# Optimization experiments

Measured on AMD Instinct MI355X. Metric: run time of the kernel, lower is better.

## Reference

```python
import jax, jax.numpy as jnp
import numpy as np

TEMPERATURE = 0.7
TOP_K = 50
TOP_P = 0.9
B, S, H, V = 2, 1024, 512, 50257


def setup_inputs() -> dict:
    key = jax.random.key(0)
    k1, k2 = jax.random.split(key)
    x = jax.random.normal(k1, (B, S, H), dtype=jnp.float32)
    # small init scale keeps logits in a realistic range so nucleus mass is spread
    W = jax.random.normal(k2, (V, H), dtype=jnp.float32) * 0.02
    b = jnp.zeros((V,), dtype=jnp.float32)
    return {"x": x, "W": W, "b": b}


def _top_k_top_p_filtering(logits):
    # --- top-k: mask everything below the k-th largest value ---
    top_k_vals = jax.lax.top_k(logits, TOP_K)[0]          # [B,S,K]
    min_top_k = top_k_vals[..., -1:]                       # [B,S,1]
    logits = jnp.where(logits < min_top_k, -jnp.inf, logits)
    # --- top-p (nucleus): sort descending, cumsum of probs, drop tail ---
    sorted_idx = jnp.argsort(-logits, axis=-1)             # descending order
    sorted_logits = jnp.take_along_axis(logits, sorted_idx, axis=-1)
    cum_probs = jnp.cumsum(jax.nn.softmax(sorted_logits, axis=-1), axis=-1)
    sorted_logits = jnp.where(cum_probs > TOP_P, -jnp.inf, sorted_logits)
    # NOTE: the original torch code does gather(sorted_logits, index=sorted_indices)
    # (forward-gather, not inverse scatter). We replicate that exact math.
    logits = jnp.take_along_axis(sorted_logits, sorted_idx, axis=-1)
    return logits


def reference(x, W, b):
    # ExampleModel: single linear projection to vocab logits [B,S,V]
    logits = jnp.einsum('bsh,vh->bsv', x, W) + b
    logits = logits / TEMPERATURE
    filtered = _top_k_top_p_filtering(logits)
    return jax.nn.softmax(filtered, axis=-1)
```

## Files before the change

### kernel.cpp

```cpp
#include <hip/hip_runtime.h>
#include <math.h>

#define TEMP 0.7f
#define TOPK 50
#define TOPP 0.9f
#define M_TOT 2048
#define K_DIM 512
#define V_DIM 50257
#define NPAD 50304
#define KP 1536
#define BM 256
#define BN 128
#define BKE 64
#define NSTEP (KP / BKE)
#define NBN (NPAD / BN)
#define NBM (M_TOT / BM)

typedef short s16x8 __attribute__((ext_vector_type(8)));
typedef float f32x4 __attribute__((ext_vector_type(4)));

#define MFMA_16x16x32_BF16(acc, va, vb) \
  asm("v_mfma_f32_16x16x32_bf16 %0, %1, %2, %0" : "+v"(acc) : "v"(va), "v"(vb))

__device__ __forceinline__ unsigned short bf16_rn(float x) {
  unsigned u = __float_as_uint(x);
  unsigned r = u + 0x7FFFu + ((u >> 16) & 1u);
  return (unsigned short)(r >> 16);
}
__device__ __forceinline__ float bf16_to_f(unsigned short h) {
  return __uint_as_float(((unsigned)h) << 16);
}
__device__ __forceinline__ unsigned f2key(float f) {
  unsigned u = __float_as_uint(f);
  return (u & 0x80000000u) ? ~u : (u | 0x80000000u);
}

#define NQX (M_TOT * (K_DIM / 4))
#define NQW (NPAD * (K_DIM / 4))
#define NZQ ((M_TOT * V_DIM) / 4)

__global__ __launch_bounds__(256) void conv_kernel(const float* __restrict__ X,
                                                   const float* __restrict__ W,
                                                   unsigned short* __restrict__ Xp,
                                                   unsigned short* __restrict__ Wp,
                                                   float* __restrict__ Z, int nzq) {
  int idx = blockIdx.x * 256 + threadIdx.x;
  if (idx >= NQX + NQW) {
    int zi = idx - (NQX + NQW);
    if (zi < nzq) {
      const f32x4 z4 = {0.f, 0.f, 0.f, 0.f};
      reinterpret_cast<f32x4*>(Z)[zi] = z4;
    }
    return;
  }
  float4 v;
  unsigned short* dst;
  size_t base;
  int mode;
  if (idx < NQX) {
    int row = idx >> 7, q = idx & 127;
    v = reinterpret_cast<const float4*>(X)[idx];
    dst = Xp;
    base = (size_t)row * KP + q * 4;
    mode = 0;
  } else {
    int wi = idx - NQX;
    int row = wi >> 7, q = wi & 127;
    v = make_float4(0.f, 0.f, 0.f, 0.f);
    if (row < V_DIM) v = reinterpret_cast<const float4*>(W)[(size_t)row * 128 + q];
    dst = Wp;
    base = (size_t)row * KP + q * 4;
    mode = 1;
  }
  float vv[4] = {v.x, v.y, v.z, v.w};
  unsigned short hi[4], lo[4];
#pragma unroll
  for (int j = 0; j < 4; ++j) {
    hi[j] = bf16_rn(vv[j]);
    lo[j] = bf16_rn(vv[j] - bf16_to_f(hi[j]));
  }
  ushort4 h4 = make_ushort4(hi[0], hi[1], hi[2], hi[3]);
  ushort4 l4 = make_ushort4(lo[0], lo[1], lo[2], lo[3]);
  *reinterpret_cast<ushort4*>(dst + base) = h4;
  if (mode == 0) {
    *reinterpret_cast<ushort4*>(dst + base + K_DIM) = h4;
    *reinterpret_cast<ushort4*>(dst + base + 2 * K_DIM) = l4;
  } else {
    *reinterpret_cast<ushort4*>(dst + base + K_DIM) = l4;
    *reinterpret_cast<ushort4*>(dst + base + 2 * K_DIM) = h4;
  }
}

#define SW 68

__global__ __launch_bounds__(512) void mfma_gemm_kernel(
    const unsigned short* __restrict__ Ap, const unsigned short* __restrict__ Bp,
    const float* __restrict__ Bv, float* __restrict__ C,
    unsigned* __restrict__ Tmax) {
  __shared__ __align__(16) unsigned char lds[49152];
  const int tid = threadIdx.x;
  const int w = tid >> 6, lane = tid & 63;
  const int bm = blockIdx.x * BM;
  const int bni = blockIdx.y;
  const int bn = bni * BN;
  const int wr = w >> 1, wc = w & 1;

  f32x4 acc[4][4] = {};

  for (int step = 0; step < NSTEP; ++step) {
    const int k0 = step * BKE;
#pragma unroll
    for (int l = 0; l < 4; ++l) {
      int pp = ((l * 512 + tid) << 4);
      int row = pp >> 7;
      int cb = (pp & 127) ^ ((row & 7) << 4);
      const unsigned short* ga = Ap + (size_t)(bm + row) * KP + k0 + (cb >> 1);
      __builtin_amdgcn_global_load_lds(
          (const __attribute__((address_space(1))) unsigned int*)ga,
          (__attribute__((address_space(3))) unsigned int*)(lds + pp), 16, 0, 0);
    }
#pragma unroll
    for (int l = 0; l < 2; ++l) {
      int pp = ((l * 512 + tid) << 4);
      int row = pp >> 7;
      int cb = (pp & 127) ^ ((row & 7) << 4);
      const unsigned short* gb = Bp + (size_t)(bn + row) * KP + k0 + (cb >> 1);
      __builtin_amdgcn_global_load_lds(
          (const __attribute__((address_space(1))) unsigned int*)gb,
          (__attribute__((address_space(3))) unsigned int*)(lds + 32768 + pp), 16, 0, 0);
    }
    __syncthreads();
#pragma unroll
    for (int kk = 0; kk < 2; ++kk) {
      const int kbyte = kk * 64 + ((lane >> 4) << 4);
      s16x8 a[4], b[4];
#pragma unroll
      for (int i = 0; i < 4; ++i) {
        int row = (wr << 6) + (i << 4) + (lane & 15);
        int byte = (row << 7) + (kbyte ^ ((row & 7) << 4));
        a[i] = *reinterpret_cast<const s16x8*>(lds + byte);
      }
#pragma unroll
      for (int j = 0; j < 4; ++j) {
        int row = (wc << 6) + (j << 4) + (lane & 15);
        int byte = (row << 7) + (kbyte ^ ((row & 7) << 4));
        b[j] = *reinterpret_cast<const s16x8*>(lds + 32768 + byte);
      }
#pragma unroll
      for (int i = 0; i < 4; ++i)
#pragma unroll
        for (int j = 0; j < 4; ++j) MFMA_16x16x32_BF16(acc[i][j], a[i], b[j]);
    }
    __syncthreads();
  }

  __syncthreads();
  float* wreg = reinterpret_cast<float*>(lds) + w * (16 * SW);
  float mx[4][4];
#pragma unroll
  for (int i = 0; i < 4; ++i)
#pragma unroll
    for (int r = 0; r < 4; ++r) mx[i][r] = -INFINITY;

#pragma unroll
  for (int i = 0; i < 4; ++i) {
#pragma unroll
    for (int j = 0; j < 4; ++j) {
      int n = bn + (wc << 6) + (j << 4) + (lane & 15);
      float bv = (n < V_DIM) ? Bv[n] : 0.f;
#pragma unroll
      for (int r = 0; r < 4; ++r) {
        float val = (acc[i][j][r] + bv) / TEMP;
        wreg[(((lane >> 4) << 2) + r) * SW + (j << 4) + (lane & 15)] = val;
        if (n < V_DIM) mx[i][r] = fmaxf(mx[i][r], val);
      }
    }
    int row = lane >> 2;
    int m = bm + (wr << 6) + (i << 4) + row;
#pragma unroll
    for (int it = 0; it < 4; ++it) {
      int c2 = ((lane & 3) << 2) + (it << 4);
      f32x4 v4 = *reinterpret_cast<const f32x4*>(wreg + row * SW + c2);
      int n4 = bn + (wc << 6) + c2;
      if (n4 + 3 < V_DIM) {
        *reinterpret_cast<f32x4*>(&C[(size_t)m * V_DIM + n4]) = v4;
      } else {
#pragma unroll
        for (int e = 0; e < 4; ++e)
          if (n4 + e < V_DIM) C[(size_t)m * V_DIM + n4 + e] = v4[e];
      }
    }
  }

  __syncthreads();
  unsigned* umax = reinterpret_cast<unsigned*>(lds);
  if (tid < BM) umax[tid] = 0;
  __syncthreads();
#pragma unroll
  for (int i = 0; i < 4; ++i) {
#pragma unroll
    for (int r = 0; r < 4; ++r) {
      float v = mx[i][r];
      v = fmaxf(v, __shfl_xor(v, 1));
      v = fmaxf(v, __shfl_xor(v, 2));
      v = fmaxf(v, __shfl_xor(v, 4));
      v = fmaxf(v, __shfl_xor(v, 8));
      if ((lane & 15) == 0)
        atomicMax(&umax[(wr << 6) + (i << 4) + ((lane >> 4) << 2) + r], f2key(v));
    }
  }
  __syncthreads();
  if (tid < BM) Tmax[(size_t)(bm + tid) * NBN + bni] = umax[tid];
}

#define CAP 1024
#define SCAP 256

__global__ __launch_bounds__(256) void select_kernel(const float* __restrict__ Lg,
                                                     float* __restrict__ C,
                                                     const unsigned* __restrict__ Tmax,
                                                     int do_zero) {
  const int row = blockIdx.x;
  const float* rowin = Lg + (size_t)row * V_DIM;
  float* rowout = C + (size_t)row * V_DIM;
  const int tid = threadIdx.x;

  __shared__ unsigned tk[NBN];
  __shared__ short ctile[NBN];
  __shared__ unsigned s_t50;
  __shared__ float cval[CAP];
  __shared__ int cidx[CAP];
  __shared__ float sval[SCAP];
  __shared__ int sidx[SCAP];
  __shared__ float pvals[SCAP];
  __shared__ int s_cnt, s_ntile, s_nsurv, s_kc;
  __shared__ float s_invZ;

  for (int i = tid; i < NBN; i += 256) tk[i] = Tmax[(size_t)row * NBN + i];
  if (tid == 0) { s_cnt = 0; s_ntile = 0; s_nsurv = 0; }
  __syncthreads();
  for (int i = tid; i < NBN; i += 256) {
    unsigned ki = tk[i];
    int r = 0;
    for (int j = 0; j < NBN; ++j) {
      unsigned kj = tk[j];
      r += (kj > ki) || (kj == ki && j < i);
    }
    if (r == TOPK - 1) s_t50 = ki;
  }
  __syncthreads();
  const unsigned t50 = s_t50;

  for (int i = tid; i < NBN; i += 256) {
    if (tk[i] >= t50) {
      int p = atomicAdd(&s_ntile, 1);
      ctile[p] = (short)i;
    }
  }
  __syncthreads();
  const int ntile = s_ntile;

  for (int e = tid; e < ntile * BN; e += 256) {
    int ti = ctile[e >> 7];
    int n = ti * BN + (e & 127);
    if (n < V_DIM) {
      float l = rowin[n];
      if (f2key(l) >= t50) {
        int p = atomicAdd(&s_cnt, 1);
        if (p < CAP) { cval[p] = l; cidx[p] = n; }
      }
    }
  }
  __syncthreads();
  const int n = min(s_cnt, CAP);

  if (do_zero) {
    const f32x4 z4 = {0.f, 0.f, 0.f, 0.f};
    const int NQ = V_DIM >> 2;
    f32x4* rp4 = reinterpret_cast<f32x4*>(rowout);
    for (int q = tid; q < NQ; q += 256) rp4[q] = z4;
    if (tid == 0) rowout[V_DIM - 1] = 0.f;
  }

  for (int i = tid; i < n; i += 256) {
    float vi = cval[i];
    int xi = cidx[i];
    int r = 0;
    for (int j = 0; j < n; ++j) {
      float vj = cval[j];
      if (vj > vi || (vj == vi && cidx[j] < xi)) ++r;
    }
    if (r < SCAP) { sval[r] = vi; sidx[r] = xi; }
  }
  __syncthreads();

  const float t = sval[TOPK - 1];
  for (int i = tid; i < n; i += 256)
    if (cval[i] >= t) atomicAdd(&s_nsurv, 1);
  __syncthreads();
  const int nsurv = min(s_nsurv, SCAP);

  const float m = sval[0];
  for (int i = tid; i < nsurv; i += 256) pvals[i] = expf(sval[i] - m);
  __syncthreads();
  if (tid == 0) {
    float Z0 = 0.f;
    for (int i = 0; i < nsurv; ++i) Z0 += pvals[i];
    float cum = 0.f;
    int kc = 0;
    float Z2 = 0.f;
    for (int i = 0; i < nsurv; ++i) {
      cum += pvals[i] / Z0;
      if (cum > TOPP) break;
      kc = i + 1;
      Z2 += pvals[i];
    }
    s_kc = kc;
    s_invZ = (kc > 0) ? (1.f / Z2) : 0.f;
  }
  __syncthreads();
  const int kc = s_kc;
  const float invZ = s_invZ;

  for (int q = tid; q < kc; q += 256) {
    int r = -1, less = 0;
    for (int s = 0; s < nsurv; ++s) {
      if (sidx[s] == q) r = s;
      if (sidx[s] < q) ++less;
    }
    int rank = (r >= 0) ? r : (nsurv + q - less);
    rowout[rank] = pvals[q] * invZ;
  }
}

extern "C" void kernel_launch(void* const* d_in, const int* in_sizes, int n_in,
                              void* d_out, int out_size, void* d_ws, size_t ws_size,
                              hipStream_t stream) {
  const float* X = (const float*)d_in[0];
  const float* W = (const float*)d_in[1];
  const float* Bv = (const float*)d_in[2];
  float* C = (float*)d_out;

  unsigned short* Xp = (unsigned short*)d_ws;
  unsigned short* Wp = Xp + (size_t)M_TOT * KP;
  unsigned* Tmax = (unsigned*)(Wp + (size_t)NPAD * KP);
  float* Lws = (float*)(Tmax + (size_t)M_TOT * NBN);

  const size_t need_big = (size_t)((char*)(Lws + (size_t)M_TOT * V_DIM) - (char*)d_ws);
  const int big = (ws_size >= need_big);

  float* Lg = big ? Lws : C;
  const int nzq = big ? NZQ : 0;

  conv_kernel<<<(NQX + NQW + nzq + 255) / 256, 256, 0, stream>>>(X, W, Xp, Wp, C, nzq);
  dim3 g(NBM, NBN);
  mfma_gemm_kernel<<<g, 512, 0, stream>>>(Xp, Wp, Bv, Lg, Tmax);
  select_kernel<<<M_TOT, 256, 0, stream>>>(Lg, C, Tmax, big ? 0 : 1);
}
```

Baseline: 638.2 us.

## Store hi/lo bf16 split once and zero output inside GEMM epilogue

The packed operands now hold only hi and lo halves (1024 columns instead of 1536 with a duplicated hi). The GEMM remaps its three K phases to compute hi*hi, hi*lo and lo*hi by offsetting into the shared layout. Zeroing of the output buffer moves from the conversion kernel into the GEMM after its main loop. Together these cut workspace writes and the extra zero-fill launch work, though the zero stores now lengthen the GEMM epilogue.

```diff
diff --git a/kernel.cpp b/kernel.cpp
--- a/kernel.cpp
+++ b/kernel.cpp
@@ -8,11 +8,11 @@
 #define K_DIM 512
 #define V_DIM 50257
 #define NPAD 50304
-#define KP 1536
+#define KP2 1024
 #define BM 256
 #define BN 128
 #define BKE 64
-#define NSTEP (KP / BKE)
+#define NSTEP 24
 #define NBN (NPAD / BN)
 #define NBM (M_TOT / BM)
 
@@ -37,40 +37,28 @@
 
 #define NQX (M_TOT * (K_DIM / 4))
 #define NQW (NPAD * (K_DIM / 4))
-#define NZQ ((M_TOT * V_DIM) / 4)
 
 __global__ __launch_bounds__(256) void conv_kernel(const float* __restrict__ X,
                                                    const float* __restrict__ W,
                                                    unsigned short* __restrict__ Xp,
-                                                   unsigned short* __restrict__ Wp,
-                                                   float* __restrict__ Z, int nzq) {
+                                                   unsigned short* __restrict__ Wp) {
   int idx = blockIdx.x * 256 + threadIdx.x;
-  if (idx >= NQX + NQW) {
-    int zi = idx - (NQX + NQW);
-    if (zi < nzq) {
-      const f32x4 z4 = {0.f, 0.f, 0.f, 0.f};
-      reinterpret_cast<f32x4*>(Z)[zi] = z4;
-    }
-    return;
-  }
   float4 v;
   unsigned short* dst;
   size_t base;
-  int mode;
   if (idx < NQX) {
     int row = idx >> 7, q = idx & 127;
     v = reinterpret_cast<const float4*>(X)[idx];
     dst = Xp;
-    base = (size_t)row * KP + q * 4;
-    mode = 0;
+    base = (size_t)row * KP2 + q * 4;
   } else {
     int wi = idx - NQX;
+    if (wi >= NQW) return;
     int row = wi >> 7, q = wi & 127;
     v = make_float4(0.f, 0.f, 0.f, 0.f);
     if (row < V_DIM) v = reinterpret_cast<const float4*>(W)[(size_t)row * 128 + q];
     dst = Wp;
-    base = (size_t)row * KP + q * 4;
-    mode = 1;
+    base = (size_t)row * KP2 + q * 4;
   }
   float vv[4] = {v.x, v.y, v.z, v.w};
   unsigned short hi[4], lo[4];
@@ -79,16 +67,8 @@
     hi[j] = bf16_rn(vv[j]);
     lo[j] = bf16_rn(vv[j] - bf16_to_f(hi[j]));
   }
-  ushort4 h4 = make_ushort4(hi[0], hi[1], hi[2], hi[3]);
-  ushort4 l4 = make_ushort4(lo[0], lo[1], lo[2], lo[3]);
-  *reinterpret_cast<ushort4*>(dst + base) = h4;
-  if (mode == 0) {
-    *reinterpret_cast<ushort4*>(dst + base + K_DIM) = h4;
-    *reinterpret_cast<ushort4*>(dst + base + 2 * K_DIM) = l4;
-  } else {
-    *reinterpret_cast<ushort4*>(dst + base + K_DIM) = l4;
-    *reinterpret_cast<ushort4*>(dst + base + 2 * K_DIM) = h4;
-  }
+  *reinterpret_cast<ushort4*>(dst + base) = make_ushort4(hi[0], hi[1], hi[2], hi[3]);
+  *reinterpret_cast<ushort4*>(dst + base + K_DIM) = make_ushort4(lo[0], lo[1], lo[2], lo[3]);
 }
 
 #define SW 68
@@ -96,7 +76,7 @@
 __global__ __launch_bounds__(512) void mfma_gemm_kernel(
     const unsigned short* __restrict__ Ap, const unsigned short* __restrict__ Bp,
     const float* __restrict__ Bv, float* __restrict__ C,
-    unsigned* __restrict__ Tmax) {
+    unsigned* __restrict__ Tmax, float* __restrict__ Cz) {
   __shared__ __align__(16) unsigned char lds[49152];
   const int tid = threadIdx.x;
   const int w = tid >> 6, lane = tid & 63;
@@ -108,13 +88,15 @@
   f32x4 acc[4][4] = {};
 
   for (int step = 0; step < NSTEP; ++step) {
-    const int k0 = step * BKE;
+    const int phase = step >> 3, kbase = (step & 7) * BKE;
+    const int kA = (phase == 2 ? 512 : 0) + kbase;
+    const int kB = (phase == 1 ? 512 : 0) + kbase;
 #pragma unroll
     for (int l = 0; l < 4; ++l) {
       int pp = ((l * 512 + tid) << 4);
       int row = pp >> 7;
       int cb = (pp & 127) ^ ((row & 7) << 4);
-      const unsigned short* ga = Ap + (size_t)(bm + row) * KP + k0 + (cb >> 1);
+      const unsigned short* ga = Ap + (size_t)(bm + row) * KP2 + kA + (cb >> 1);
       __builtin_amdgcn_global_load_lds(
           (const __attribute__((address_space(1))) unsigned int*)ga,
           (__attribute__((address_space(3))) unsigned int*)(lds + pp), 16, 0, 0);
@@ -124,7 +106,7 @@
       int pp = ((l * 512 + tid) << 4);
       int row = pp >> 7;
       int cb = (pp & 127) ^ ((row & 7) << 4);
-      const unsigned short* gb = Bp + (size_t)(bn + row) * KP + k0 + (cb >> 1);
+      const unsigned short* gb = Bp + (size_t)(bn + row) * KP2 + kB + (cb >> 1);
       __builtin_amdgcn_global_load_lds(
           (const __attribute__((address_space(1))) unsigned int*)gb,
           (__attribute__((address_space(3))) unsigned int*)(lds + 32768 + pp), 16, 0, 0);
@@ -152,6 +134,24 @@
         for (int j = 0; j < 4; ++j) MFMA_16x16x32_BF16(acc[i][j], a[i], b[j]);
     }
     __syncthreads();
+  }
+
+  if (Cz) {
+    const f32x4 z4 = {0.f, 0.f, 0.f, 0.f};
+#pragma unroll
+    for (int l = 0; l < 16; ++l) {
+      int e = l * 512 + tid;
+      int rq = e >> 5, cq = e & 31;
+      int m = bm + rq;
+      int n4 = bn + (cq << 2);
+      if (n4 + 3 < V_DIM) {
+        *reinterpret_cast<f32x4*>(&Cz[(size_t)m * V_DIM + n4]) = z4;
+      } else {
+#pragma unroll
+        for (int ee = 0; ee < 4; ++ee)
+          if (n4 + ee < V_DIM) Cz[(size_t)m * V_DIM + n4 + ee] = 0.f;
+      }
+    }
   }
 
   __syncthreads();
@@ -342,18 +342,17 @@
   float* C = (float*)d_out;
 
   unsigned short* Xp = (unsigned short*)d_ws;
-  unsigned short* Wp = Xp + (size_t)M_TOT * KP;
-  unsigned* Tmax = (unsigned*)(Wp + (size_t)NPAD * KP);
+  unsigned short* Wp = Xp + (size_t)M_TOT * KP2;
+  unsigned* Tmax = (unsigned*)(Wp + (size_t)NPAD * KP2);
   float* Lws = (float*)(Tmax + (size_t)M_TOT * NBN);
 
   const size_t need_big = (size_t)((char*)(Lws + (size_t)M_TOT * V_DIM) - (char*)d_ws);
   const int big = (ws_size >= need_big);
 
   float* Lg = big ? Lws : C;
-  const int nzq = big ? NZQ : 0;
-
-  conv_kernel<<<(NQX + NQW + nzq + 255) / 256, 256, 0, stream>>>(X, W, Xp, Wp, C, nzq);
+
+  conv_kernel<<<(NQX + NQW + 255) / 256, 256, 0, stream>>>(X, W, Xp, Wp);
   dim3 g(NBM, NBN);
-  mfma_gemm_kernel<<<g, 512, 0, stream>>>(Xp, Wp, Bv, Lg, Tmax);
+  mfma_gemm_kernel<<<g, 512, 0, stream>>>(Xp, Wp, Bv, Lg, Tmax, big ? C : nullptr);
   select_kernel<<<M_TOT, 256, 0, stream>>>(Lg, C, Tmax, big ? 0 : 1);
 }
```

Measured after the change: 652.1 us. +2.2%, slower.
